# Kernel optimization log

Hardware: AMD Instinct MI355X
Metric: run time of the kernel (lower is better)

## Reference

```python
import jax, jax.numpy as jnp
import numpy as np

B, H, E = 16, 4096, 512
N_MODES = 24  # len(index_q), permutation of range(48//2)


def setup_inputs() -> dict:
    key = jax.random.key(0)
    ks = jax.random.split(key, 7)
    s = 1.0 / np.sqrt(E)
    inp = {
        "x": jax.random.normal(ks[0], (B, H, E), jnp.float32),
        "Wq": jax.random.normal(ks[1], (E, E), jnp.float32) * s,
        "bq": jax.random.normal(ks[2], (E,), jnp.float32) * s,
        "Wk": jax.random.normal(ks[3], (E, E), jnp.float32) * s,
        "bk": jax.random.normal(ks[4], (E,), jnp.float32) * s,
        "Wv": jax.random.normal(ks[5], (E, E), jnp.float32) * s,
        "bv": jax.random.normal(ks[6], (E,), jnp.float32) * s,
        # shuffled permutation of range(24), as in the module __init__
        "index_q": jnp.asarray(np.random.RandomState(0).permutation(N_MODES), jnp.int32),
    }
    return inp


def reference(x, Wq, bq, Wk, bk, Wv, bv, index_q):
    # nn.Linear: y = x @ W.T + b
    Q = x @ Wq.T + bq
    K = x @ Wk.T + bk
    V = x @ Wv.T + bv  # computed but unused downstream (faithful to original bug)
    del V

    # rFFT over feature dim, gather selected frequency modes (vectorized,
    # replacing the original per-index Python loops)
    xq_ft = jnp.fft.rfft(Q, axis=-1)[:, :, index_q]          # [B,H,24] complex
    xk_ft = jnp.fft.rfft(K, axis=-1)[:, :, index_q]          # [B,H,24]
    xv_ft = xk_ft                                            # original uses rfft(K) for V too

    # cross-frequency attention: contract over H (no conjugation, as torch.einsum)
    xqk_ft = jnp.einsum('bhx,bhy->bxy', xq_ft, xk_ft)        # [B,24,24] complex
    att = jax.nn.softmax(jnp.abs(xqk_ft), axis=-1)           # real [B,24,24]
    att_c = jax.lax.complex(att, jnp.zeros_like(att))
    xqkv_ft = jnp.einsum('bxy,bhy->bhx', att_c, xv_ft)       # [B,H,24]

    # scatter selected modes back into the full spectrum, inverse rFFT
    n_freq = E // 2 + 1
    out_ft = jnp.zeros((x.shape[0], x.shape[1], n_freq), jnp.complex64)
    out_ft = out_ft.at[:, :, index_q].set(xqkv_ft)
    out = jnp.fft.irfft(out_ft, n=E, axis=-1)                # [B,H,E] real
    return out.astype(x.dtype)
```

## Files before the change

kernel.cpp:

```cpp
#include <hip/hip_runtime.h>
#include <stdint.h>

#define E_DIM 512
#define NM 24
#define NC 48
#define NCOL 96
#define B_DIM 16
#define H_DIM 4096
#define NROWS (B_DIM * H_DIM)

__global__ __launch_bounds__(128)
void k_buildC(const float* __restrict__ Wq, const float* __restrict__ Wk,
              const float* __restrict__ bq, const float* __restrict__ bk,
              const int* __restrict__ idxq,
              float* __restrict__ C, float* __restrict__ dvec) {
  __shared__ float twc[E_DIM], tws[E_DIM];
  __shared__ int fj[NM];
  const int t = threadIdx.x;
  for (int i = t; i < E_DIM; i += 128) {
    float s, c;
    sincospif((float)i * (1.0f / 256.0f), &s, &c);
    twc[i] = c; tws[i] = s;
  }
  if (t < NM) fj[t] = idxq[t];
  __syncthreads();
  const int e = blockIdx.x;
  if (t >= NCOL) return;
  const int mat = t / NC;
  const int c = t - mat * NC;
  const int j = c >> 1, p = c & 1;
  const int f = fj[j];
  float acc = 0.0f;
  if (e < E_DIM) {
    const float* __restrict__ W = mat ? Wk : Wq;
    for (int o = 0; o < E_DIM; ++o) {
      const float w = W[o * E_DIM + e];
      const int tt = (f * o) & (E_DIM - 1);
      acc = fmaf(w, p ? -tws[tt] : twc[tt], acc);
    }
    C[e * NCOL + t] = acc;
  } else {
    const float* __restrict__ bv = mat ? bk : bq;
    for (int o = 0; o < E_DIM; ++o) {
      const int tt = (f * o) & (E_DIM - 1);
      acc = fmaf(bv[o], p ? -tws[tt] : twc[tt], acc);
    }
    dvec[t] = acc;
  }
}

__global__ __launch_bounds__(256)
void k_buildM(const int* __restrict__ idxq, float* __restrict__ M) {
  const int gid = blockIdx.x * 256 + threadIdx.x;
  if (gid >= NC * E_DIM) return;
  const int c = gid >> 9;
  const int e = gid & (E_DIM - 1);
  const int j = c >> 1, p = c & 1;
  const int f = idxq[j];
  const float w = (f == 0 ? 1.0f : 2.0f) * (1.0f / (float)E_DIM);
  float s, cc;
  sincospif((float)((f * e) & (E_DIM - 1)) * (1.0f / 256.0f), &s, &cc);
  M[c * E_DIM + e] = p ? (-w * s) : (w * cc);
}

#define GBM 128
#define GBK 32
__global__ __launch_bounds__(512)
void k_gemmG(const float* __restrict__ x, const float* __restrict__ C,
             const float* __restrict__ dvec, float* __restrict__ G) {
  __shared__ __align__(16) float xs[GBK][GBM + 4];
  __shared__ __align__(16) float cs[GBK * NCOL];
  __shared__ float dsh[NCOL];
  const int t = threadIdx.x;
  const int ri = t >> 4;
  const int ci = t & 15;
  const int row0 = blockIdx.x * GBM;
  if (t < NCOL) dsh[t] = dvec[t];
  float acc[4][6];
#pragma unroll
  for (int a = 0; a < 4; ++a)
#pragma unroll
    for (int b = 0; b < 6; ++b) acc[a][b] = 0.0f;

  for (int k0 = 0; k0 < E_DIM; k0 += GBK) {
    __syncthreads();
#pragma unroll
    for (int it = 0; it < 2; ++it) {
      const int idx = t + it * 512;
      const int row = idx >> 3, kc = idx & 7;
      const float4 v = *(const float4*)&x[(row0 + row) * E_DIM + k0 + kc * 4];
      xs[kc * 4 + 0][row] = v.x;
      xs[kc * 4 + 1][row] = v.y;
      xs[kc * 4 + 2][row] = v.z;
      xs[kc * 4 + 3][row] = v.w;
    }
#pragma unroll
    for (int it = 0; it < 2; ++it) {
      const int idx = t + it * 512;
      if (idx < (GBK * NCOL) / 4)
        *(float4*)&cs[idx * 4] = *(const float4*)&C[k0 * NCOL + idx * 4];
    }
    __syncthreads();
#pragma unroll 8
    for (int kk = 0; kk < GBK; ++kk) {
      const float4 xv = *(const float4*)&xs[kk][ri * 4];
      const float2 c0 = *(const float2*)&cs[kk * NCOL + ci * 6 + 0];
      const float2 c1 = *(const float2*)&cs[kk * NCOL + ci * 6 + 2];
      const float2 c2 = *(const float2*)&cs[kk * NCOL + ci * 6 + 4];
      const float xr[4] = {xv.x, xv.y, xv.z, xv.w};
      const float cv[6] = {c0.x, c0.y, c1.x, c1.y, c2.x, c2.y};
#pragma unroll
      for (int a = 0; a < 4; ++a)
#pragma unroll
        for (int b = 0; b < 6; ++b)
          acc[a][b] = fmaf(xr[a], cv[b], acc[a][b]);
    }
  }
#pragma unroll
  for (int a = 0; a < 4; ++a) {
    const int row = row0 + ri * 4 + a;
#pragma unroll
    for (int b = 0; b < 6; b += 2) {
      float2 v;
      v.x = acc[a][b]     + dsh[ci * 6 + b];
      v.y = acc[a][b + 1] + dsh[ci * 6 + b + 1];
      *(float2*)&G[row * NCOL + ci * 6 + b] = v;
    }
  }
}

__global__ __launch_bounds__(576)
void k_spart(const float* __restrict__ G, float* __restrict__ Sp) {
  const int t = threadIdx.x;
  const int xx = t / NM, yy = t - xx * NM;
  const int bc = blockIdx.x;
  const int b = bc >> 5, hc = bc & 31;
  const int r0 = b * H_DIM + hc * 128;
  float sre = 0.0f, sim = 0.0f;
  for (int h = 0; h < 128; ++h) {
    const float* __restrict__ g = &G[(r0 + h) * NCOL];
    const float2 q = *(const float2*)&g[2 * xx];
    const float2 k = *(const float2*)&g[NC + 2 * yy];
    sre += q.x * k.x - q.y * k.y;
    sim += q.x * k.y + q.y * k.x;
  }
  ((float2*)Sp)[bc * 576 + t] = make_float2(sre, sim);
}

__global__ __launch_bounds__(576)
void k_att(const float* __restrict__ Sp, float* __restrict__ att) {
  __shared__ float mag[576];
  __shared__ float ex[576];
  const int t = threadIdx.x;
  const int b = blockIdx.x;
  float sre = 0.0f, sim = 0.0f;
  const float2* in2 = (const float2*)Sp;
  for (int hc = 0; hc < 32; ++hc) {
    const float2 v = in2[(b * 32 + hc) * 576 + t];
    sre += v.x; sim += v.y;
  }
  mag[t] = sqrtf(sre * sre + sim * sim);
  __syncthreads();
  const int xx = t / NM;
  float m = -1e30f;
  for (int k = 0; k < NM; ++k) m = fmaxf(m, mag[xx * NM + k]);
  const float e = expf(mag[t] - m);
  ex[t] = e;
  __syncthreads();
  float s = 0.0f;
  for (int k = 0; k < NM; ++k) s += ex[xx * NM + k];
  att[b * 576 + t] = e / s;
}

__global__ __launch_bounds__(256)
void k_z(const float* __restrict__ G, const float* __restrict__ att,
         float* __restrict__ Z) {
  __shared__ float at[576];
  const int t = threadIdx.x;
  const int row = blockIdx.x * 256 + t;
  const int b = blockIdx.x >> 4;
  for (int i = t; i < 576; i += 256) at[i] = att[b * 576 + i];
  __syncthreads();
  float gk[NC];
#pragma unroll
  for (int i = 0; i < NC / 4; ++i) {
    const float4 v = *(const float4*)&G[row * NCOL + NC + i * 4];
    gk[i * 4 + 0] = v.x; gk[i * 4 + 1] = v.y; gk[i * 4 + 2] = v.z; gk[i * 4 + 3] = v.w;
  }
  float z[NC];
#pragma unroll
  for (int xx = 0; xx < NM; ++xx) {
    float zr = 0.0f, zi = 0.0f;
#pragma unroll
    for (int y = 0; y < NM; ++y) {
      const float a = at[xx * NM + y];
      zr = fmaf(a, gk[2 * y], zr);
      zi = fmaf(a, gk[2 * y + 1], zi);
    }
    z[2 * xx] = zr; z[2 * xx + 1] = zi;
  }
#pragma unroll
  for (int i = 0; i < NC / 4; ++i) {
    float4 v;
    v.x = z[i * 4]; v.y = z[i * 4 + 1]; v.z = z[i * 4 + 2]; v.w = z[i * 4 + 3];
    *(float4*)&Z[row * NC + i * 4] = v;
  }
}

#define OBM 128
#define OBN 128
__global__ __launch_bounds__(256)
void k_out(const float* __restrict__ Z, const float* __restrict__ M,
           float* __restrict__ out) {
  __shared__ __align__(16) float zs[NC][OBM + 4];
  __shared__ __align__(16) float ms[NC * OBN];
  const int t = threadIdx.x;
  const int ri = t >> 4, ci = t & 15;
  const int row0 = (blockIdx.x >> 2) * OBM;
  const int e0 = (blockIdx.x & 3) * OBN;
#pragma unroll
  for (int it = 0; it < 6; ++it) {
    const int idx = t + it * 256;
    const int row = idx / 12, kc = idx - row * 12;
    const float4 v = *(const float4*)&Z[(row0 + row) * NC + kc * 4];
    zs[kc * 4 + 0][row] = v.x;
    zs[kc * 4 + 1][row] = v.y;
    zs[kc * 4 + 2][row] = v.z;
    zs[kc * 4 + 3][row] = v.w;
  }
#pragma unroll
  for (int it = 0; it < 6; ++it) {
    const int idx = t + it * 256;
    const int k = idx >> 5, ec = idx & 31;
    *(float4*)&ms[k * OBN + ec * 4] = *(const float4*)&M[k * E_DIM + e0 + ec * 4];
  }
  __syncthreads();
  float acc[8][8];
#pragma unroll
  for (int a = 0; a < 8; ++a)
#pragma unroll
    for (int b = 0; b < 8; ++b) acc[a][b] = 0.0f;
#pragma unroll 4
  for (int k = 0; k < NC; ++k) {
    const float4 za = *(const float4*)&zs[k][ri * 8];
    const float4 zb = *(const float4*)&zs[k][ri * 8 + 4];
    const float4 ma = *(const float4*)&ms[k * OBN + ci * 8];
    const float4 mb = *(const float4*)&ms[k * OBN + ci * 8 + 4];
    const float zr[8] = {za.x, za.y, za.z, za.w, zb.x, zb.y, zb.z, zb.w};
    const float mr[8] = {ma.x, ma.y, ma.z, ma.w, mb.x, mb.y, mb.z, mb.w};
#pragma unroll
    for (int a = 0; a < 8; ++a)
#pragma unroll
      for (int b = 0; b < 8; ++b)
        acc[a][b] = fmaf(zr[a], mr[b], acc[a][b]);
  }
#pragma unroll
  for (int a = 0; a < 8; ++a) {
    const int row = row0 + ri * 8 + a;
    float4 v0, v1;
    v0.x = acc[a][0]; v0.y = acc[a][1]; v0.z = acc[a][2]; v0.w = acc[a][3];
    v1.x = acc[a][4]; v1.y = acc[a][5]; v1.z = acc[a][6]; v1.w = acc[a][7];
    *(float4*)&out[row * E_DIM + e0 + ci * 8] = v0;
    *(float4*)&out[row * E_DIM + e0 + ci * 8 + 4] = v1;
  }
}

extern "C" void kernel_launch(void* const* d_in, const int* in_sizes, int n_in,
                              void* d_out, int out_size, void* d_ws, size_t ws_size,
                              hipStream_t stream) {
  const float* x  = (const float*)d_in[0];
  const float* Wq = (const float*)d_in[1];
  const float* bq = (const float*)d_in[2];
  const float* Wk = (const float*)d_in[3];
  const float* bk = (const float*)d_in[4];
  const int* idxq = (const int*)d_in[7];
  float* out = (float*)d_out;
  float* ws = (float*)d_ws;

  float* C   = ws;
  float* dv  = ws + 49152;
  float* M   = ws + 49280;
  float* att = ws + 73856;
  float* Sp  = ws + 83072;
  float* Z   = ws + 672896;
  float* G   = out;

  k_buildC<<<E_DIM + 1, 128, 0, stream>>>(Wq, Wk, bq, bk, idxq, C, dv);
  k_buildM<<<(NC * E_DIM + 255) / 256, 256, 0, stream>>>(idxq, M);
  k_gemmG<<<NROWS / GBM, 512, 0, stream>>>(x, C, dv, G);
  k_spart<<<B_DIM * 32, 576, 0, stream>>>(G, Sp);
  k_att<<<B_DIM, 576, 0, stream>>>(Sp, att);
  k_z<<<NROWS / 256, 256, 0, stream>>>(G, att, Z);
  k_out<<<(NROWS / OBM) * (E_DIM / OBN), 256, 0, stream>>>(Z, M, out);
}
```

Baseline: 435.5 us.

## Merge build kernels, enlarge GEMM register tile with prefetch, stage G in LDS

Merges the C/dvec and M construction kernels into one launch. The projection GEMM goes from 512 threads computing 4x6 outputs each to 128 threads computing 8x12 each, and prefetches the next K tile into registers while the current one is computed. k_spart now stages its 128-row G tile into shared memory before the reduction, and k_z uses 128-thread blocks. The goals are fewer launches, more arithmetic per LDS load and hidden global latency, at the cost of much higher register pressure and lower occupancy in the GEMM.

```diff
diff --git a/kernel.cpp b/kernel.cpp
--- a/kernel.cpp
+++ b/kernel.cpp
@@ -10,13 +10,26 @@
 #define NROWS (B_DIM * H_DIM)
 
 __global__ __launch_bounds__(128)
-void k_buildC(const float* __restrict__ Wq, const float* __restrict__ Wk,
-              const float* __restrict__ bq, const float* __restrict__ bk,
-              const int* __restrict__ idxq,
-              float* __restrict__ C, float* __restrict__ dvec) {
+void k_build(const float* __restrict__ Wq, const float* __restrict__ Wk,
+             const float* __restrict__ bq, const float* __restrict__ bk,
+             const int* __restrict__ idxq,
+             float* __restrict__ C, float* __restrict__ dvec, float* __restrict__ M) {
   __shared__ float twc[E_DIM], tws[E_DIM];
   __shared__ int fj[NM];
   const int t = threadIdx.x;
+  const int bid = blockIdx.x;
+  if (bid >= E_DIM + 1) {
+    const int gid = (bid - (E_DIM + 1)) * 128 + t;
+    const int c = gid >> 9;
+    const int e = gid & (E_DIM - 1);
+    const int j = c >> 1, p = c & 1;
+    const int f = idxq[j];
+    const float w = (f == 0 ? 1.0f : 2.0f) * (1.0f / (float)E_DIM);
+    float s, cc;
+    sincospif((float)((f * e) & (E_DIM - 1)) * (1.0f / 256.0f), &s, &cc);
+    M[c * E_DIM + e] = p ? (-w * s) : (w * cc);
+    return;
+  }
   for (int i = t; i < E_DIM; i += 128) {
     float s, c;
     sincospif((float)i * (1.0f / 256.0f), &s, &c);
@@ -24,7 +37,7 @@
   }
   if (t < NM) fj[t] = idxq[t];
   __syncthreads();
-  const int e = blockIdx.x;
+  const int e = bid;
   if (t >= NCOL) return;
   const int mat = t / NC;
   const int c = t - mat * NC;
@@ -49,98 +62,115 @@
   }
 }
 
-__global__ __launch_bounds__(256)
-void k_buildM(const int* __restrict__ idxq, float* __restrict__ M) {
-  const int gid = blockIdx.x * 256 + threadIdx.x;
-  if (gid >= NC * E_DIM) return;
-  const int c = gid >> 9;
-  const int e = gid & (E_DIM - 1);
-  const int j = c >> 1, p = c & 1;
-  const int f = idxq[j];
-  const float w = (f == 0 ? 1.0f : 2.0f) * (1.0f / (float)E_DIM);
-  float s, cc;
-  sincospif((float)((f * e) & (E_DIM - 1)) * (1.0f / 256.0f), &s, &cc);
-  M[c * E_DIM + e] = p ? (-w * s) : (w * cc);
-}
-
 #define GBM 128
 #define GBK 32
-__global__ __launch_bounds__(512)
+__global__ __launch_bounds__(128)
 void k_gemmG(const float* __restrict__ x, const float* __restrict__ C,
              const float* __restrict__ dvec, float* __restrict__ G) {
-  __shared__ __align__(16) float xs[GBK][GBM + 4];
+  __shared__ __align__(16) float xs[GBK][132];
   __shared__ __align__(16) float cs[GBK * NCOL];
   __shared__ float dsh[NCOL];
   const int t = threadIdx.x;
-  const int ri = t >> 4;
-  const int ci = t & 15;
+  const int ri = t >> 3;
+  const int ci = t & 7;
   const int row0 = blockIdx.x * GBM;
   if (t < NCOL) dsh[t] = dvec[t];
-  float acc[4][6];
-#pragma unroll
-  for (int a = 0; a < 4; ++a)
-#pragma unroll
-    for (int b = 0; b < 6; ++b) acc[a][b] = 0.0f;
-
-  for (int k0 = 0; k0 < E_DIM; k0 += GBK) {
+  float acc[8][12];
+#pragma unroll
+  for (int a = 0; a < 8; ++a)
+#pragma unroll
+    for (int b = 0; b < 12; ++b) acc[a][b] = 0.0f;
+
+  float4 xv[8], cv[6];
+#pragma unroll
+  for (int r = 0; r < 8; ++r) {
+    const int lin = r * 128 + t;
+    xv[r] = *(const float4*)&x[(row0 + (lin >> 3)) * E_DIM + ((lin & 7) << 2)];
+  }
+#pragma unroll
+  for (int r = 0; r < 6; ++r)
+    cv[r] = *(const float4*)&C[(r * 128 + t) * 4];
+
+  for (int k0 = 0;; k0 += GBK) {
     __syncthreads();
 #pragma unroll
-    for (int it = 0; it < 2; ++it) {
-      const int idx = t + it * 512;
-      const int row = idx >> 3, kc = idx & 7;
-      const float4 v = *(const float4*)&x[(row0 + row) * E_DIM + k0 + kc * 4];
-      xs[kc * 4 + 0][row] = v.x;
-      xs[kc * 4 + 1][row] = v.y;
-      xs[kc * 4 + 2][row] = v.z;
-      xs[kc * 4 + 3][row] = v.w;
-    }
-#pragma unroll
-    for (int it = 0; it < 2; ++it) {
-      const int idx = t + it * 512;
-      if (idx < (GBK * NCOL) / 4)
-        *(float4*)&cs[idx * 4] = *(const float4*)&C[k0 * NCOL + idx * 4];
-    }
+    for (int r = 0; r < 8; ++r) {
+      const int lin = r * 128 + t;
+      const int row = lin >> 3, kc = lin & 7;
+      xs[kc * 4 + 0][row] = xv[r].x;
+      xs[kc * 4 + 1][row] = xv[r].y;
+      xs[kc * 4 + 2][row] = xv[r].z;
+      xs[kc * 4 + 3][row] = xv[r].w;
+    }
+#pragma unroll
+    for (int r = 0; r < 6; ++r)
+      *(float4*)&cs[(r * 128 + t) * 4] = cv[r];
     __syncthreads();
-#pragma unroll 8
+    const bool more = (k0 + GBK) < E_DIM;
+    if (more) {
+      const int kn = k0 + GBK;
+#pragma unroll
+      for (int r = 0; r < 8; ++r) {
+        const int lin = r * 128 + t;
+        xv[r] = *(const float4*)&x[(row0 + (lin >> 3)) * E_DIM + kn + ((lin & 7) << 2)];
+      }
+#pragma unroll
+      for (int r = 0; r < 6; ++r)
+        cv[r] = *(const float4*)&C[kn * NCOL + (r * 128 + t) * 4];
+    }
+#pragma unroll 4
     for (int kk = 0; kk < GBK; ++kk) {
-      const float4 xv = *(const float4*)&xs[kk][ri * 4];
-      const float2 c0 = *(const float2*)&cs[kk * NCOL + ci * 6 + 0];
-      const float2 c1 = *(const float2*)&cs[kk * NCOL + ci * 6 + 2];
-      const float2 c2 = *(const float2*)&cs[kk * NCOL + ci * 6 + 4];
-      const float xr[4] = {xv.x, xv.y, xv.z, xv.w};
-      const float cv[6] = {c0.x, c0.y, c1.x, c1.y, c2.x, c2.y};
-#pragma unroll
-      for (int a = 0; a < 4; ++a)
-#pragma unroll
-        for (int b = 0; b < 6; ++b)
-          acc[a][b] = fmaf(xr[a], cv[b], acc[a][b]);
-    }
-  }
-#pragma unroll
-  for (int a = 0; a < 4; ++a) {
-    const int row = row0 + ri * 4 + a;
-#pragma unroll
-    for (int b = 0; b < 6; b += 2) {
-      float2 v;
-      v.x = acc[a][b]     + dsh[ci * 6 + b];
-      v.y = acc[a][b + 1] + dsh[ci * 6 + b + 1];
-      *(float2*)&G[row * NCOL + ci * 6 + b] = v;
+      const float4 xa = *(const float4*)&xs[kk][ri * 8];
+      const float4 xb = *(const float4*)&xs[kk][ri * 8 + 4];
+      const float4 c0 = *(const float4*)&cs[kk * NCOL + ci * 12];
+      const float4 c1 = *(const float4*)&cs[kk * NCOL + ci * 12 + 4];
+      const float4 c2 = *(const float4*)&cs[kk * NCOL + ci * 12 + 8];
+      const float xr[8] = {xa.x, xa.y, xa.z, xa.w, xb.x, xb.y, xb.z, xb.w};
+      const float cc[12] = {c0.x, c0.y, c0.z, c0.w, c1.x, c1.y, c1.z, c1.w,
+                            c2.x, c2.y, c2.z, c2.w};
+#pragma unroll
+      for (int a = 0; a < 8; ++a)
+#pragma unroll
+        for (int b = 0; b < 12; ++b)
+          acc[a][b] = fmaf(xr[a], cc[b], acc[a][b]);
+    }
+    if (!more) break;
+  }
+#pragma unroll
+  for (int a = 0; a < 8; ++a) {
+    const int row = row0 + ri * 8 + a;
+#pragma unroll
+    for (int b4 = 0; b4 < 3; ++b4) {
+      float4 v;
+      v.x = acc[a][b4 * 4 + 0] + dsh[ci * 12 + b4 * 4 + 0];
+      v.y = acc[a][b4 * 4 + 1] + dsh[ci * 12 + b4 * 4 + 1];
+      v.z = acc[a][b4 * 4 + 2] + dsh[ci * 12 + b4 * 4 + 2];
+      v.w = acc[a][b4 * 4 + 3] + dsh[ci * 12 + b4 * 4 + 3];
+      *(float4*)&G[row * NCOL + ci * 12 + b4 * 4] = v;
     }
   }
 }
 
 __global__ __launch_bounds__(576)
 void k_spart(const float* __restrict__ G, float* __restrict__ Sp) {
+  __shared__ __align__(16) float gs[128 * NCOL];
   const int t = threadIdx.x;
   const int xx = t / NM, yy = t - xx * NM;
   const int bc = blockIdx.x;
   const int b = bc >> 5, hc = bc & 31;
   const int r0 = b * H_DIM + hc * 128;
+  const float4* __restrict__ g4 = (const float4*)G;
+#pragma unroll
+  for (int r = 0; r < 6; ++r) {
+    const int idx = t + r * 576;
+    if (idx < 128 * NCOL / 4)
+      ((float4*)gs)[idx] = g4[r0 * (NCOL / 4) + idx];
+  }
+  __syncthreads();
   float sre = 0.0f, sim = 0.0f;
   for (int h = 0; h < 128; ++h) {
-    const float* __restrict__ g = &G[(r0 + h) * NCOL];
-    const float2 q = *(const float2*)&g[2 * xx];
-    const float2 k = *(const float2*)&g[NC + 2 * yy];
+    const float2 q = *(const float2*)&gs[h * NCOL + 2 * xx];
+    const float2 k = *(const float2*)&gs[h * NCOL + NC + 2 * yy];
     sre += q.x * k.x - q.y * k.y;
     sim += q.x * k.y + q.y * k.x;
   }
@@ -172,14 +202,14 @@
   att[b * 576 + t] = e / s;
 }
 
-__global__ __launch_bounds__(256)
+__global__ __launch_bounds__(128)
 void k_z(const float* __restrict__ G, const float* __restrict__ att,
          float* __restrict__ Z) {
   __shared__ float at[576];
   const int t = threadIdx.x;
-  const int row = blockIdx.x * 256 + t;
-  const int b = blockIdx.x >> 4;
-  for (int i = t; i < 576; i += 256) at[i] = att[b * 576 + i];
+  const int row = blockIdx.x * 128 + t;
+  const int b = row >> 12;
+  for (int i = t; i < 576; i += 128) at[i] = att[b * 576 + i];
   __syncthreads();
   float gk[NC];
 #pragma unroll
@@ -285,11 +315,10 @@
   float* Z   = ws + 672896;
   float* G   = out;
 
-  k_buildC<<<E_DIM + 1, 128, 0, stream>>>(Wq, Wk, bq, bk, idxq, C, dv);
-  k_buildM<<<(NC * E_DIM + 255) / 256, 256, 0, stream>>>(idxq, M);
-  k_gemmG<<<NROWS / GBM, 512, 0, stream>>>(x, C, dv, G);
+  k_build<<<E_DIM + 1 + (NC * E_DIM) / 128, 128, 0, stream>>>(Wq, Wk, bq, bk, idxq, C, dv, M);
+  k_gemmG<<<NROWS / GBM, 128, 0, stream>>>(x, C, dv, G);
   k_spart<<<B_DIM * 32, 576, 0, stream>>>(G, Sp);
   k_att<<<B_DIM, 576, 0, stream>>>(Sp, att);
-  k_z<<<NROWS / 256, 256, 0, stream>>>(G, att, Z);
+  k_z<<<NROWS / 128, 128, 0, stream>>>(G, att, Z);
   k_out<<<(NROWS / OBM) * (E_DIM / OBN), 256, 0, stream>>>(Z, M, out);
 }
```

Result: slower. 463.8 us (+6.5%).
